# Kernel tuning notes

Hardware: AMD Instinct MI355X
Metric: run time of the kernel (lower is better)

The kernel has to match this reference:

```python
import jax, jax.numpy as jnp
import numpy as np

M, B, D, Z, CH, K = 3, 8192, 2000, 256, 2, 40
F = Z // CH  # 128


def setup_inputs() -> dict:
    key = jax.random.key(0)
    ks = jax.random.split(key, 10)
    x = jax.random.normal(ks[0], (M, B, D), jnp.float32)
    # Stacked per-modality encoder weights (Linear+ReLU stack, dropout=0)
    enc_w0 = jax.random.normal(ks[1], (M, D, 1024), jnp.float32) * 0.02
    enc_b0 = jnp.zeros((M, 1024), jnp.float32)
    enc_w1 = jax.random.normal(ks[2], (M, 1024, 512), jnp.float32) * 0.02
    enc_b1 = jnp.zeros((M, 512), jnp.float32)
    enc_w2 = jax.random.normal(ks[3], (M, 512, Z), jnp.float32) * 0.02
    enc_b2 = jnp.zeros((M, Z), jnp.float32)
    # Attention params (torch.randn init in the original)
    aff = jax.random.normal(ks[4], (3, F, F), jnp.float32)      # C(3)=3 bilinear mats
    W = jax.random.normal(ks[5], (M, K, F), jnp.float32)
    Wh = jax.random.normal(ks[6], (M, M, K, 1), jnp.float32)
    return dict(x=x, enc_w0=enc_w0, enc_b0=enc_b0, enc_w1=enc_w1, enc_b1=enc_b1,
                enc_w2=enc_w2, enc_b2=enc_b2, aff=aff, W=W, Wh=Wh)


def reference(x, enc_w0, enc_b0, enc_w1, enc_b1, enc_w2, enc_b2, aff, W, Wh):
    # Encoders: Linear+ReLU x3, batched over modalities
    h = jax.nn.relu(jnp.einsum('mbd,mdh->mbh', x, enc_w0) + enc_b0[:, None, :])
    h = jax.nn.relu(jnp.einsum('mbd,mdh->mbh', h, enc_w1) + enc_b1[:, None, :])
    z = jax.nn.relu(jnp.einsum('mbd,mdh->mbh', h, enc_w2) + enc_b2[:, None, :])  # (M,B,Z)
    m, b = z.shape[0], z.shape[1]
    t = z.reshape(m, b, F, CH)  # (M,B,128,2), same layout as torch reshape

    # aff_weight index bookkeeping exactly as the original python loops:
    # per-row i, index starts at 0 and increments only after an i<j use.
    aff_idx = {}
    for i in range(m):
        idx = 0
        for j in range(i, m):
            aff_idx[(i, j)] = idx
            if i < j:
                idx += 1

    # affinity[i][j] = t_i^T @ aff @ t_j  -> (B,CH,CH)
    afm = {}
    for i in range(m):
        for j in range(i, m):
            afm[(i, j)] = jnp.einsum('bfc,fg,bgd->bcd', t[i], aff[aff_idx[(i, j)]], t[j])

    Wt = jnp.einsum('mkf,mbfc->mbkc', W, t)  # W[i] @ t_i, (M,B,K,CH)

    H = {}
    for i in range(m):
        for j in range(m):
            if i <= j:
                H[(i, j)] = jnp.tanh(Wt[j] + jnp.einsum('bkc,bcd->bkd', Wt[i], afm[(i, j)]))
            else:
                aff_ij = jnp.swapaxes(afm[(j, i)], 1, 2)
                H[(i, j)] = jnp.tanh(Wt[i] + jnp.einsum('bkc,bcd->bkd', Wt[j], aff_ij))

    outs = []
    for i in range(m):
        for j in range(m):
            if i != j:
                # A = softmax(W_h^T @ H) over the channel axis -> (B,CH)
                a = jax.nn.softmax(jnp.einsum('k,bkc->bc', Wh[i, j, :, 0], H[(i, j)]), axis=-1)
                outs.append((a[:, None, :] * t[i]).reshape(b, Z))
    concat_data = jnp.concatenate(outs, axis=1)  # (B, M*(M-1)*Z)
    return z, concat_data
```

## Files before the change

kernel.cpp:

```cpp
#include <hip/hip_runtime.h>

#define DEVI __device__ __forceinline__

typedef _Float16 f16;
typedef _Float16 f16x8 __attribute__((ext_vector_type(8)));
typedef float f32x4 __attribute__((ext_vector_type(4)));
typedef unsigned int u32;
typedef unsigned long long u64;

#define MM 3
#define BBATCH 8192
#define DDIM 2000
#define ZDIM 256
#define KATT 40
#define K0P 2048
#define N0 1024
#define N1 512
#define N2 256

typedef __attribute__((address_space(1))) u32 gu32;
typedef __attribute__((address_space(3))) u32 lu32;

DEVI void async16(const void* g, void* l) {
  __builtin_amdgcn_global_load_lds((const gu32*)g, (lu32*)l, 16, 0, 0);
}

__global__ void k_convx(const float* __restrict__ x, f16* __restrict__ xh) {
  const long long nch = (long long)MM * BBATCH * (K0P / 8);
  for (long long idx = (long long)blockIdx.x * blockDim.x + threadIdx.x; idx < nch;
       idx += (long long)gridDim.x * blockDim.x) {
    int c8 = (int)(idx & 255);
    long long row = idx >> 8;
    union { f16 h[8]; f16x8 v; } u;
    if (c8 < DDIM / 8) {
      const float* src = x + row * DDIM + c8 * 8;
      float4 a = *reinterpret_cast<const float4*>(src);
      float4 b = *reinterpret_cast<const float4*>(src + 4);
      u.h[0] = (f16)a.x; u.h[1] = (f16)a.y; u.h[2] = (f16)a.z; u.h[3] = (f16)a.w;
      u.h[4] = (f16)b.x; u.h[5] = (f16)b.y; u.h[6] = (f16)b.z; u.h[7] = (f16)b.w;
    } else {
      for (int j = 0; j < 8; ++j) u.h[j] = (f16)0.f;
    }
    *reinterpret_cast<f16x8*>(xh + row * K0P + c8 * 8) = u.v;
  }
}

__global__ void k_wt(const float* __restrict__ w, f16* __restrict__ wt, int K, int Kpad, int N) {
  __shared__ float tile[32][33];
  int m = blockIdx.z;
  int k0 = blockIdx.x * 32, n0 = blockIdx.y * 32;
  const float* wm = w + (long long)m * K * N;
  f16* wtm = wt + (long long)m * N * Kpad;
  for (int p = 0; p < 4; ++p) {
    int idx = threadIdx.x + p * 256;
    int kk = idx >> 5, nn = idx & 31;
    float v = 0.f;
    if (k0 + kk < K) v = wm[(long long)(k0 + kk) * N + n0 + nn];
    tile[kk][nn] = v;
  }
  __syncthreads();
  for (int p = 0; p < 4; ++p) {
    int idx = threadIdx.x + p * 256;
    int nn = idx >> 5, kk = idx & 31;
    wtm[(long long)(n0 + nn) * Kpad + k0 + kk] = (f16)tile[kk][nn];
  }
}

__global__ void k_convsmall(const float* __restrict__ aff, const float* __restrict__ W,
                            f16* __restrict__ affH, f16* __restrict__ WH) {
  int idx = blockIdx.x * 256 + threadIdx.x;
  if (idx < 2 * 128 * 128) affH[idx] = (f16)aff[idx];
  if (idx < 3 * 64 * 128) {
    int m = idx >> 13;
    int k = (idx >> 7) & 63;
    int f = idx & 127;
    WH[idx] = (k < KATT) ? (f16)W[(m * KATT + k) * 128 + f] : (f16)0.f;
  }
}

template <int OUTF16>
__global__ __launch_bounds__(256, 2) void k_gemm(const f16* __restrict__ A,
                                                 const f16* __restrict__ BT,
                                                 const float* __restrict__ bias,
                                                 f16* __restrict__ outh,
                                                 float* __restrict__ outf,
                                                 f16* __restrict__ tH, int K, int N) {
  __shared__ f16 As[128 * 64];
  __shared__ f16 Bs[128 * 64];
  const int m = blockIdx.z;
  const int gm0 = blockIdx.y * 128;
  const int gn0 = blockIdx.x * 128;
  const int tid = threadIdx.x;
  const int wave = tid >> 6, lane = tid & 63;
  const int wr = wave >> 1, wc = wave & 1;

  const f16* Am = A + (long long)m * BBATCH * K;
  const f16* Bm = BT + (long long)m * N * K;

  const int srow = wave * 32 + (lane >> 3);
  const int sslot = (lane & 7) ^ (lane >> 3);
  const f16* aSrc = Am + (long long)(gm0 + srow) * K + sslot * 8;
  const f16* bSrc = Bm + (long long)(gn0 + srow) * K + sslot * 8;
  char* AsB = (char*)As;
  char* BsB = (char*)Bs;

  f32x4 zero = {0.f, 0.f, 0.f, 0.f};
  f32x4 acc[4][4];
  for (int i = 0; i < 4; ++i)
    for (int j = 0; j < 4; ++j) acc[i][j] = zero;

  for (int kt = 0; kt < K; kt += 64) {
    if (kt) __syncthreads();
#pragma unroll
    for (int q = 0; q < 4; ++q) {
      async16(aSrc + (long long)q * 8 * K + kt, AsB + (wave * 32 + q * 8) * 128);
      async16(bSrc + (long long)q * 8 * K + kt, BsB + (wave * 32 + q * 8) * 128);
    }
    __syncthreads();
#pragma unroll
    for (int ks = 0; ks < 2; ++ks) {
      f16x8 af[4], bf[4];
#pragma unroll
      for (int i = 0; i < 4; ++i) {
        int row = wr * 64 + i * 16 + (lane & 15);
        int slot = (ks * 4 + (lane >> 4)) ^ (row & 7);
        af[i] = *reinterpret_cast<const f16x8*>(AsB + row * 128 + slot * 16);
      }
#pragma unroll
      for (int j = 0; j < 4; ++j) {
        int row = wc * 64 + j * 16 + (lane & 15);
        int slot = (ks * 4 + (lane >> 4)) ^ (row & 7);
        bf[j] = *reinterpret_cast<const f16x8*>(BsB + row * 128 + slot * 16);
      }
#pragma unroll
      for (int i = 0; i < 4; ++i)
#pragma unroll
        for (int j = 0; j < 4; ++j)
          acc[i][j] = __builtin_amdgcn_mfma_f32_16x16x32_f16(af[i], bf[j], acc[i][j], 0, 0, 0);
    }
  }

  const int rowl = (lane >> 4) * 4;
  const int coll = lane & 15;
  for (int j = 0; j < 4; ++j) {
    int col = gn0 + wc * 64 + j * 16 + coll;
    float bv = bias[m * N + col];
    for (int i = 0; i < 4; ++i) {
      int row0 = gm0 + wr * 64 + i * 16 + rowl;
      for (int r = 0; r < 4; ++r) {
        float v = acc[i][j][r] + bv;
        v = v > 0.f ? v : 0.f;
        if constexpr (OUTF16) {
          outh[((long long)m * BBATCH + row0 + r) * N + col] = (f16)v;
        } else {
          outf[((long long)m * BBATCH + row0 + r) * N + col] = v;
          tH[((long long)(m * BBATCH + row0 + r) * 2 + (col & 1)) * 128 + (col >> 1)] = (f16)v;
        }
      }
    }
  }
}

__global__ __launch_bounds__(256, 2) void k_sg(const f16* __restrict__ tH,
                                               const f16* __restrict__ affH,
                                               const f16* __restrict__ WH,
                                               f16* __restrict__ u, float* __restrict__ WtG) {
  __shared__ f16 As[128 * 128];
  __shared__ f16 Bs[128 * 128];
  const int zb = blockIdx.z;
  const int gm0 = blockIdx.y * 128;
  const bool isU = (zb < 3);
  const int p = isU ? zb : zb - 3;
  const int src = isU ? ((p == 0) ? 1 : 2) : p;
  const f16* Am = tH + (long long)src * 16384 * 128;
  const f16* Bm;
  int brows;
  if (isU) {
    int km = (p == 1) ? 1 : 0;
    Bm = affH + km * 128 * 128;
    brows = 128;
  } else {
    Bm = WH + p * 64 * 128;
    brows = 64;
  }

  const int tid = threadIdx.x;
  const int wave = tid >> 6, lane = tid & 63;
  const int wr = wave >> 1, wc = wave & 1;
  char* AsB = (char*)As;
  char* BsB = (char*)Bs;

#pragma unroll
  for (int q = 0; q < 8; ++q) {
    int sb = q * 4 + wave;
    int row = sb * 4 + (lane >> 4);
    int lsl = (lane & 15) ^ (row & 7);
    async16(Am + (long long)(gm0 + row) * 128 + lsl * 8, AsB + sb * 1024);
    if (sb * 4 < brows)
      async16(Bm + (long long)row * 128 + lsl * 8, BsB + sb * 1024);
  }
  if (brows == 64) {
    f16x8 z8 = {};
    for (int idx = tid; idx < 1024; idx += 256) {
      int row = 64 + (idx >> 4), sl = idx & 15;
      *reinterpret_cast<f16x8*>(BsB + row * 256 + sl * 16) = z8;
    }
  }
  __syncthreads();

  f32x4 zero = {0.f, 0.f, 0.f, 0.f};
  f32x4 acc[4][4];
  for (int i = 0; i < 4; ++i)
    for (int j = 0; j < 4; ++j) acc[i][j] = zero;

#pragma unroll
  for (int ks = 0; ks < 4; ++ks) {
    f16x8 af[4], bf[4];
#pragma unroll
    for (int i = 0; i < 4; ++i) {
      int row = wr * 64 + i * 16 + (lane & 15);
      int slot = (ks * 4 + (lane >> 4)) ^ (row & 7);
      af[i] = *reinterpret_cast<const f16x8*>(AsB + row * 256 + slot * 16);
    }
#pragma unroll
    for (int j = 0; j < 4; ++j) {
      int row = wc * 64 + j * 16 + (lane & 15);
      int slot = (ks * 4 + (lane >> 4)) ^ (row & 7);
      bf[j] = *reinterpret_cast<const f16x8*>(BsB + row * 256 + slot * 16);
    }
#pragma unroll
    for (int i = 0; i < 4; ++i)
#pragma unroll
      for (int j = 0; j < 4; ++j)
        acc[i][j] = __builtin_amdgcn_mfma_f32_16x16x32_f16(af[i], bf[j], acc[i][j], 0, 0, 0);
  }

  const int rowl = (lane >> 4) * 4;
  const int coll = lane & 15;
  if (isU) {
    for (int j = 0; j < 4; ++j) {
      int col = wc * 64 + j * 16 + coll;
      for (int i = 0; i < 4; ++i) {
        int row0 = gm0 + wr * 64 + i * 16 + rowl;
        for (int r = 0; r < 4; ++r)
          u[((long long)p * 16384 + row0 + r) * 128 + col] = (f16)acc[i][j][r];
      }
    }
  } else if (wc == 0) {
    for (int j = 0; j < 4; ++j) {
      int col = j * 16 + coll;
      for (int i = 0; i < 4; ++i) {
        int row0 = gm0 + wr * 64 + i * 16 + rowl;
        for (int r = 0; r < 4; ++r)
          WtG[((long long)p * 16384 + row0 + r) * 64 + col] = acc[i][j][r];
      }
    }
  }
}

DEVI float dot128(const f16* __restrict__ a, const f16* __restrict__ b) {
  float s = 0.f;
#pragma unroll
  for (int ch = 0; ch < 16; ++ch) {
    f16x8 av = *reinterpret_cast<const f16x8*>(a + ch * 8);
    f16x8 bv = *reinterpret_cast<const f16x8*>(b + ch * 8);
#pragma unroll
    for (int q = 0; q < 8; ++q) s += (float)av[q] * (float)bv[q];
  }
  return s;
}

DEVI float ftanh(float x) {
  x = fminf(fmaxf(x, -15.f), 15.f);
  float t = __expf(-2.f * x);
  return (1.f - t) / (1.f + t);
}

#define BB 32
__global__ void k_tail(const float* __restrict__ z, const f16* __restrict__ tH,
                       const f16* __restrict__ u, const float* __restrict__ WtG,
                       const float* __restrict__ Wh, float* __restrict__ out) {
  __shared__ float aa[BB][6][2];
  const int tid = threadIdx.x;
  const int bbase = blockIdx.x * BB;

  if (tid < BB * 6) {
    int bb = tid / 6, q = tid % 6;
    int b = bbase + bb;
    int i = q >> 1;
    int j = (q & 1) ? ((i == 2) ? 1 : 2) : ((i == 0) ? 1 : 0);
    int a = i < j ? i : j;
    int b2 = i < j ? j : i;
    int pidx = a + b2 - 1;
    bool trans = (i > j);

    float afm[2][2];
#pragma unroll
    for (int c = 0; c < 2; ++c)
#pragma unroll
      for (int d = 0; d < 2; ++d)
        afm[c][d] = dot128(tH + ((long long)(a * BBATCH + b) * 2 + c) * 128,
                           u + ((long long)pidx * 16384 + b * 2 + d) * 128);

    float m00, m01, m10, m11;
    if (!trans) { m00 = afm[0][0]; m01 = afm[0][1]; m10 = afm[1][0]; m11 = afm[1][1]; }
    else        { m00 = afm[0][0]; m01 = afm[1][0]; m10 = afm[0][1]; m11 = afm[1][1]; }

    const float* wb0 = WtG + ((long long)b2 * 16384 + b * 2 + 0) * 64;
    const float* wb1 = WtG + ((long long)b2 * 16384 + b * 2 + 1) * 64;
    const float* wa0 = WtG + ((long long)a * 16384 + b * 2 + 0) * 64;
    const float* wa1 = WtG + ((long long)a * 16384 + b * 2 + 1) * 64;
    const float* wh = Wh + (i * 3 + j) * KATT;
    float s0 = 0.f, s1 = 0.f;
    for (int k = 0; k < KATT; ++k) {
      float a0v = wa0[k], a1v = wa1[k];
      float h0 = ftanh(wb0[k] + a0v * m00 + a1v * m10);
      float h1 = ftanh(wb1[k] + a0v * m01 + a1v * m11);
      float w = wh[k];
      s0 += w * h0;
      s1 += w * h1;
    }
    float mx = fmaxf(s0, s1);
    float e0 = __expf(s0 - mx), e1 = __expf(s1 - mx);
    float inv = 1.f / (e0 + e1);
    aa[bb][q][0] = e0 * inv;
    aa[bb][q][1] = e1 * inv;
  }
  __syncthreads();

  for (int idx = tid; idx < BB * 6 * 256; idx += 256) {
    int zz = idx & 255;
    int r = idx >> 8;
    int q = r % 6;
    int bb = r / 6;
    int iM = q >> 1;
    float av = aa[bb][q][zz & 1];
    float tv = z[((long long)iM * BBATCH + bbase + bb) * ZDIM + zz];
    out[(long long)(bbase + bb) * 1536 + q * 256 + zz] = av * tv;
  }
}

extern "C" void kernel_launch(void* const* d_in, const int* in_sizes, int n_in, void* d_out,
                              int out_size, void* d_ws, size_t ws_size, hipStream_t stream) {
  const float* x = (const float*)d_in[0];
  const float* w0 = (const float*)d_in[1];
  const float* b0 = (const float*)d_in[2];
  const float* w1 = (const float*)d_in[3];
  const float* b1 = (const float*)d_in[4];
  const float* w2 = (const float*)d_in[5];
  const float* b2 = (const float*)d_in[6];
  const float* aff = (const float*)d_in[7];
  const float* W = (const float*)d_in[8];
  const float* Wh = (const float*)d_in[9];
  float* zout = (float*)d_out;
  float* cout = zout + (long long)MM * BBATCH * ZDIM;

  char* ws = (char*)d_ws;
  size_t off = 0;
  auto alloc = [&](size_t bytes) {
    char* p = ws + off;
    off += (bytes + 255) & ~(size_t)255;
    return p;
  };
  f16* xh = (f16*)alloc((size_t)MM * BBATCH * K0P * 2);
  f16* wT0 = (f16*)alloc((size_t)MM * N0 * K0P * 2);
  f16* wT1 = (f16*)alloc((size_t)MM * N1 * N0 * 2);
  f16* wT2 = (f16*)alloc((size_t)MM * N2 * N1 * 2);
  f16* h0 = (f16*)alloc((size_t)MM * BBATCH * N0 * 2);
  f16* h1 = (f16*)alloc((size_t)MM * BBATCH * N1 * 2);
  f16* affH = (f16*)alloc((size_t)2 * 128 * 128 * 2);
  f16* WH = (f16*)alloc((size_t)3 * 64 * 128 * 2);
  if (ws_size < off) return;

  f16* tH = (f16*)xh;
  f16* u = (f16*)((char*)xh + (size_t)3 * 16384 * 128 * 2);
  float* WtG = (float*)((char*)xh + (size_t)2 * 3 * 16384 * 128 * 2);

  k_convx<<<4096, 256, 0, stream>>>(x, xh);
  k_convsmall<<<128, 256, 0, stream>>>(aff, W, affH, WH);
  k_wt<<<dim3(K0P / 32, N0 / 32, 3), 256, 0, stream>>>(w0, wT0, DDIM, K0P, N0);
  k_wt<<<dim3(N0 / 32, N1 / 32, 3), 256, 0, stream>>>(w1, wT1, N0, N0, N1);
  k_wt<<<dim3(N1 / 32, N2 / 32, 3), 256, 0, stream>>>(w2, wT2, N1, N1, N2);
  k_gemm<1><<<dim3(N0 / 128, BBATCH / 128, 3), 256, 0, stream>>>(xh, wT0, b0, h0, nullptr, nullptr, K0P, N0);
  k_gemm<1><<<dim3(N1 / 128, BBATCH / 128, 3), 256, 0, stream>>>(h0, wT1, b1, h1, nullptr, nullptr, N0, N1);
  k_gemm<0><<<dim3(N2 / 128, BBATCH / 128, 3), 256, 0, stream>>>(h1, wT2, b2, nullptr, zout, tH, N1, N2);
  k_sg<<<dim3(1, 128, 6), 256, 0, stream>>>(tH, affH, WH, u, WtG);
  k_tail<<<256, 256, 0, stream>>>(zout, tH, u, WtG, Wh, cout);
}
```

Baseline: 314.3 us.

## Add 256x128-tile triple-buffered GEMM with 8 waves and XCD-aware block swizzle

Adds a new encoder GEMM kernel that uses 512 threads and a 256x128 output tile. Global-to-LDS loads are triple-buffered and split into two phases that interleave with MFMA compute under barriers and priority hints. Block indices are remapped so that adjacent tiles land on the same XCD, which should improve L2 reuse. The aim is to hide memory latency and raise MFMA utilisation in the three dense layers. In exchange it needs 144KB of dynamic LDS, which limits occupancy, and it keeps the old kernel as a fallback in case the attribute set fails.

```diff
diff --git a/kernel.cpp b/kernel.cpp
--- a/kernel.cpp
+++ b/kernel.cpp
@@ -147,6 +147,145 @@
     float bv = bias[m * N + col];
     for (int i = 0; i < 4; ++i) {
       int row0 = gm0 + wr * 64 + i * 16 + rowl;
+      for (int r = 0; r < 4; ++r) {
+        float v = acc[i][j][r] + bv;
+        v = v > 0.f ? v : 0.f;
+        if constexpr (OUTF16) {
+          outh[((long long)m * BBATCH + row0 + r) * N + col] = (f16)v;
+        } else {
+          outf[((long long)m * BBATCH + row0 + r) * N + col] = v;
+          tH[((long long)(m * BBATCH + row0 + r) * 2 + (col & 1)) * 128 + (col >> 1)] = (f16)v;
+        }
+      }
+    }
+  }
+}
+
+template <int OUTF16>
+__global__ __launch_bounds__(512, 2) void k_gemm3(const f16* __restrict__ A,
+                                                  const f16* __restrict__ BT,
+                                                  const float* __restrict__ bias,
+                                                  f16* __restrict__ outh,
+                                                  float* __restrict__ outf,
+                                                  f16* __restrict__ tH, int K, int N) {
+  extern __shared__ char lds[];
+  const int lin = blockIdx.x + gridDim.x * (blockIdx.y + gridDim.y * blockIdx.z);
+  const int cpx = (gridDim.x * gridDim.y * gridDim.z) >> 3;
+  const int swz = (lin & 7) * cpx + (lin >> 3);
+  const int bx = swz % gridDim.x;
+  const int rest = swz / gridDim.x;
+  const int by = rest % gridDim.y;
+  const int m = rest / gridDim.y;
+
+  const int gm0 = by * 256;
+  const int gn0 = bx * 128;
+  const int tid = threadIdx.x;
+  const int wave = tid >> 6, lane = tid & 63;
+  const int wr = wave >> 2, wcq = wave & 3;
+  (void)wr; (void)wcq;
+  const int wR = wave >> 1;
+  const int wC = wave & 1;
+
+  const f16* Am = A + (long long)m * BBATCH * K;
+  const f16* Bm = BT + (long long)m * N * K;
+
+  const int srow = tid >> 3;
+  const int slog = (tid & 7) ^ (srow & 7);
+  const f16* aSrc = Am + (long long)(gm0 + srow) * K + slog * 8;
+  const f16* bSrc = Bm + (long long)(gn0 + srow) * K + slog * 8;
+
+  auto stageA = [&](int bq, int kt) {
+    char* rg = lds + bq * 49152;
+#pragma unroll
+    for (int p = 0; p < 3; ++p)
+      async16(aSrc + (long long)p * 64 * K + kt, rg + p * 8192 + wave * 1024);
+  };
+  auto stageB = [&](int bq, int kt) {
+    char* rg = lds + bq * 49152;
+    async16(aSrc + (long long)3 * 64 * K + kt, rg + 3 * 8192 + wave * 1024);
+#pragma unroll
+    for (int p = 0; p < 2; ++p)
+      async16(bSrc + (long long)p * 64 * K + kt, rg + 32768 + p * 8192 + wave * 1024);
+  };
+  auto ldA = [&](const char* buf, int i, int ks) -> f16x8 {
+    int row = wR * 64 + i * 16 + (lane & 15);
+    int slot = (ks * 4 + (lane >> 4)) ^ (row & 7);
+    return *reinterpret_cast<const f16x8*>(buf + row * 128 + slot * 16);
+  };
+  auto ldB = [&](const char* buf, int j, int ks) -> f16x8 {
+    int row = wC * 64 + j * 16 + (lane & 15);
+    int slot = (ks * 4 + (lane >> 4)) ^ (row & 7);
+    return *reinterpret_cast<const f16x8*>(buf + 32768 + row * 128 + slot * 16);
+  };
+
+  f32x4 zero = {0.f, 0.f, 0.f, 0.f};
+  f32x4 acc[4][4];
+#pragma unroll
+  for (int i = 0; i < 4; ++i)
+#pragma unroll
+    for (int j = 0; j < 4; ++j) acc[i][j] = zero;
+
+  const int NT = K >> 6;
+  stageA(0, 0); stageB(0, 0);
+  stageA(1, 64); stageB(1, 64);
+  asm volatile("s_waitcnt vmcnt(6)" ::: "memory");
+  __builtin_amdgcn_s_barrier();
+
+  for (int t = 0; t < NT; ++t) {
+    const char* buf = lds + (t % 3) * 49152;
+    const int bq2 = (t + 2) % 3;
+    const int kt2 = (t + 2) << 6;
+    const bool st = (t + 2 < NT);
+    f16x8 bf[2][4], af[2][2];
+#pragma unroll
+    for (int ks = 0; ks < 2; ++ks) {
+#pragma unroll
+      for (int j = 0; j < 4; ++j) bf[ks][j] = ldB(buf, j, ks);
+#pragma unroll
+      for (int i = 0; i < 2; ++i) af[ks][i] = ldA(buf, i, ks);
+    }
+    if (st) stageA(bq2, kt2);
+    __builtin_amdgcn_s_barrier();
+    __builtin_amdgcn_s_setprio(1);
+#pragma unroll
+    for (int ks = 0; ks < 2; ++ks)
+#pragma unroll
+      for (int i = 0; i < 2; ++i)
+#pragma unroll
+        for (int j = 0; j < 4; ++j)
+          acc[i][j] = __builtin_amdgcn_mfma_f32_16x16x32_f16(af[ks][i], bf[ks][j], acc[i][j], 0, 0, 0);
+    __builtin_amdgcn_s_setprio(0);
+    __builtin_amdgcn_s_barrier();
+#pragma unroll
+    for (int ks = 0; ks < 2; ++ks)
+#pragma unroll
+      for (int i = 0; i < 2; ++i) af[ks][i] = ldA(buf, 2 + i, ks);
+    if (st) stageB(bq2, kt2);
+    __builtin_amdgcn_s_barrier();
+    __builtin_amdgcn_s_setprio(1);
+#pragma unroll
+    for (int ks = 0; ks < 2; ++ks)
+#pragma unroll
+      for (int i = 0; i < 2; ++i)
+#pragma unroll
+        for (int j = 0; j < 4; ++j)
+          acc[2 + i][j] = __builtin_amdgcn_mfma_f32_16x16x32_f16(af[ks][i], bf[ks][j], acc[2 + i][j], 0, 0, 0);
+    __builtin_amdgcn_s_setprio(0);
+    if (t < NT - 2) {
+      asm volatile("s_waitcnt vmcnt(6)" ::: "memory");
+    } else if (t == NT - 2) {
+      asm volatile("s_waitcnt vmcnt(0)" ::: "memory");
+    }
+    __builtin_amdgcn_s_barrier();
+  }
+
+  const int rowl = (lane >> 4) * 4;
+  const int coll = lane & 15;
+  for (int j = 0; j < 4; ++j) {
+    int col = gn0 + wC * 64 + j * 16 + coll;
+    float bv = bias[m * N + col];
+    for (int i = 0; i < 4; ++i) {
+      int row0 = gm0 + wR * 64 + i * 16 + rowl;
       for (int r = 0; r < 4; ++r) {
         float v = acc[i][j][r] + bv;
         v = v > 0.f ? v : 0.f;
@@ -381,9 +520,22 @@
   k_wt<<<dim3(K0P / 32, N0 / 32, 3), 256, 0, stream>>>(w0, wT0, DDIM, K0P, N0);
   k_wt<<<dim3(N0 / 32, N1 / 32, 3), 256, 0, stream>>>(w1, wT1, N0, N0, N1);
   k_wt<<<dim3(N1 / 32, N2 / 32, 3), 256, 0, stream>>>(w2, wT2, N1, N1, N2);
-  k_gemm<1><<<dim3(N0 / 128, BBATCH / 128, 3), 256, 0, stream>>>(xh, wT0, b0, h0, nullptr, nullptr, K0P, N0);
-  k_gemm<1><<<dim3(N1 / 128, BBATCH / 128, 3), 256, 0, stream>>>(h0, wT1, b1, h1, nullptr, nullptr, N0, N1);
-  k_gemm<0><<<dim3(N2 / 128, BBATCH / 128, 3), 256, 0, stream>>>(h1, wT2, b2, nullptr, zout, tH, N1, N2);
+
+  const int LDS3 = 3 * 49152;
+  static_assert(3 * 49152 <= 160 * 1024, "LDS budget");
+  hipError_t e1 = hipFuncSetAttribute(reinterpret_cast<const void*>(&k_gemm3<1>),
+                                      hipFuncAttributeMaxDynamicSharedMemorySize, LDS3);
+  hipError_t e2 = hipFuncSetAttribute(reinterpret_cast<const void*>(&k_gemm3<0>),
+                                      hipFuncAttributeMaxDynamicSharedMemorySize, LDS3);
+  if (e1 == hipSuccess && e2 == hipSuccess) {
+    k_gemm3<1><<<dim3(N0 / 128, BBATCH / 256, 3), 512, LDS3, stream>>>(xh, wT0, b0, h0, nullptr, nullptr, K0P, N0);
+    k_gemm3<1><<<dim3(N1 / 128, BBATCH / 256, 3), 512, LDS3, stream>>>(h0, wT1, b1, h1, nullptr, nullptr, N0, N1);
+    k_gemm3<0><<<dim3(N2 / 128, BBATCH / 256, 3), 512, LDS3, stream>>>(h1, wT2, b2, nullptr, zout, tH, N1, N2);
+  } else {
+    k_gemm<1><<<dim3(N0 / 128, BBATCH / 128, 3), 256, 0, stream>>>(xh, wT0, b0, h0, nullptr, nullptr, K0P, N0);
+    k_gemm<1><<<dim3(N1 / 128, BBATCH / 128, 3), 256, 0, stream>>>(h0, wT1, b1, h1, nullptr, nullptr, N0, N1);
+    k_gemm<0><<<dim3(N2 / 128, BBATCH / 128, 3), 256, 0, stream>>>(h1, wT2, b2, nullptr, zout, tH, N1, N2);
+  }
   k_sg<<<dim3(1, 128, 6), 256, 0, stream>>>(tH, affH, WH, u, WtG);
   k_tail<<<256, 256, 0, stream>>>(zout, tH, u, WtG, Wh, cout);
 }
```

Result: faster. 305.6 us (-2.8%).

## Add 256x256-tile eight-wave pipelined GEMM for encoder layers

Applied to the files above, without the earlier changes.

Adds a new encoder GEMM kernel with 256x256 output tiles and 512 threads. It uses 128KB of double-buffered dynamic LDS filled by async global-to-LDS loads, split into four staged quarter-phases with MFMA priority boosts. Block indices are swizzled across XCDs, and the three modalities are folded into the grid's y dimension. The goal is more data reuse per tile and better overlap of loads with matrix math. The cost is fewer blocks per layer, notably only 96 blocks for the last layer, and heavy LDS and register use that limits occupancy. The old kernel stays as a fallback if setting the LDS attribute fails.

```diff
diff --git a/kernel.cpp b/kernel.cpp
--- a/kernel.cpp
+++ b/kernel.cpp
@@ -155,6 +155,156 @@
         } else {
           outf[((long long)m * BBATCH + row0 + r) * N + col] = v;
           tH[((long long)(m * BBATCH + row0 + r) * 2 + (col & 1)) * 128 + (col >> 1)] = (f16)v;
+        }
+      }
+    }
+  }
+}
+
+
+#define LDA_FRAGS(QM)                                                            \
+  _Pragma("unroll") for (int ks = 0; ks < 2; ++ks)                               \
+  _Pragma("unroll") for (int mf = 0; mf < 4; ++mf) {                             \
+    const int row_ = (QM)*128 + wrB + mf * 16 + lrow;                            \
+    af[ks][mf] = *reinterpret_cast<const f16x8*>(bufA + row_ * 128 + sl16[ks]);  \
+  }
+
+#define LDB_FRAGS(QN)                                                            \
+  _Pragma("unroll") for (int ks = 0; ks < 2; ++ks)                               \
+  _Pragma("unroll") for (int nf = 0; nf < 2; ++nf) {                             \
+    const int row_ = (QN)*128 + wcB + nf * 16 + lrow;                            \
+    bf[ks][QN][nf] = *reinterpret_cast<const f16x8*>(bufB + row_ * 128 + sl16[ks]); \
+  }
+
+#define DO_MFMA(QI, QN)                                                          \
+  __builtin_amdgcn_s_setprio(1);                                                 \
+  _Pragma("unroll") for (int ks = 0; ks < 2; ++ks)                               \
+  _Pragma("unroll") for (int mf = 0; mf < 4; ++mf)                               \
+  _Pragma("unroll") for (int nf = 0; nf < 2; ++nf)                               \
+    acc[QI][mf * 2 + nf] = __builtin_amdgcn_mfma_f32_16x16x32_f16(                \
+        af[ks][mf], bf[ks][QN][nf], acc[QI][mf * 2 + nf], 0, 0, 0);              \
+  __builtin_amdgcn_s_setprio(0);
+
+#define SYNCV(VMN)                                         \
+  asm volatile("s_waitcnt vmcnt(" #VMN ")" ::: "memory");  \
+  __builtin_amdgcn_s_barrier();
+
+#define LGKM0                                              \
+  asm volatile("s_waitcnt lgkmcnt(0)" ::: "memory");       \
+  __builtin_amdgcn_sched_barrier(0);
+
+#define ENDBAR __builtin_amdgcn_s_barrier();
+
+template <int OUTF16>
+__global__ __launch_bounds__(512, 2) void k_gemm8(const f16* __restrict__ A,
+                                                  const f16* __restrict__ BT,
+                                                  const float* __restrict__ bias,
+                                                  f16* __restrict__ outh,
+                                                  float* __restrict__ outf,
+                                                  f16* __restrict__ tH, int K, int N) {
+  extern __shared__ char lds[];
+  const int lin = blockIdx.y * gridDim.x + blockIdx.x;
+  const int cpx = (gridDim.x * gridDim.y) >> 3;
+  const int swz = (lin & 7) * cpx + (lin >> 3);
+  const int bx = swz % gridDim.x;
+  const int byy = swz / gridDim.x;
+  const int m = byy >> 5;
+  const int gm0 = (byy & 31) * 256;
+  const int gn0 = bx * 256;
+
+  const int tid = threadIdx.x;
+  const int wave = tid >> 6, lane = tid & 63;
+  const int wrB = (wave >> 2) * 64;
+  const int wcB = (wave & 3) * 32;
+  const int lrow = lane & 15;
+  int sl16[2];
+#pragma unroll
+  for (int ks = 0; ks < 2; ++ks) sl16[ks] = (((ks * 4) + (lane >> 4)) ^ (lane & 7)) * 16;
+
+  const f16* Am = A + (long long)m * BBATCH * K;
+  const f16* Bm = BT + (long long)m * N * K;
+  const int srow = tid >> 3;
+  const int slog = (tid & 7) ^ (srow & 7);
+
+  auto stage = [&](int t, int hsel) {
+    const int isB = (hsel == 1 || hsel == 2) ? 1 : 0;
+    const int h = (hsel == 2 || hsel == 3) ? 1 : 0;
+    const long long grow = (long long)(isB ? gn0 : gm0) + h * 128 + srow;
+    const f16* src = (isB ? Bm : Am) + grow * K + ((long long)t << 6) + slog * 8;
+    char* dst = lds + ((t & 1) << 16) + isB * 32768 + h * 16384 + srow * 128 + (tid & 7) * 16;
+    async16(src, dst);
+    async16(src + (long long)64 * K, dst + 8192);
+  };
+
+  f16x8 af[2][4];
+  f16x8 bf[2][2][2];
+  f32x4 acc[4][8];
+  f32x4 zero = {0.f, 0.f, 0.f, 0.f};
+#pragma unroll
+  for (int qi = 0; qi < 4; ++qi)
+#pragma unroll
+    for (int f = 0; f < 8; ++f) acc[qi][f] = zero;
+
+  const int NT = K >> 6;
+  stage(0, 0); stage(0, 1); stage(0, 2); stage(0, 3);
+
+  for (int t = 0; t < NT - 1; ++t) {
+    const char* bufA = lds + ((t & 1) << 16);
+    const char* bufB = bufA + 32768;
+    stage(t + 1, 0);
+    SYNCV(6)
+    LDA_FRAGS(0) LDB_FRAGS(0) LGKM0
+    DO_MFMA(0, 0) ENDBAR
+    stage(t + 1, 1);
+    SYNCV(6)
+    LDB_FRAGS(1) LGKM0
+    DO_MFMA(1, 1) ENDBAR
+    stage(t + 1, 2);
+    SYNCV(6)
+    LDA_FRAGS(1) LGKM0
+    DO_MFMA(2, 1) ENDBAR
+    stage(t + 1, 3);
+    DO_MFMA(3, 0)
+  }
+  {
+    const int t = NT - 1;
+    const char* bufA = lds + ((t & 1) << 16);
+    const char* bufB = bufA + 32768;
+    SYNCV(4)
+    LDA_FRAGS(0) LDB_FRAGS(0) LGKM0
+    DO_MFMA(0, 0) ENDBAR
+    SYNCV(2)
+    LDB_FRAGS(1) LGKM0
+    DO_MFMA(1, 1) ENDBAR
+    SYNCV(0)
+    LDA_FRAGS(1) LGKM0
+    DO_MFMA(2, 1) ENDBAR
+    DO_MFMA(3, 0)
+  }
+
+  const int rowl = (lane >> 4) * 4;
+  const int coll = lane & 15;
+#pragma unroll
+  for (int qi = 0; qi < 4; ++qi) {
+    const int qm = (qi >= 2) ? 1 : 0;
+    const int qn = (qi == 1 || qi == 2) ? 1 : 0;
+#pragma unroll
+    for (int nf = 0; nf < 2; ++nf) {
+      int col = gn0 + qn * 128 + wcB + nf * 16 + coll;
+      float bv = bias[m * N + col];
+#pragma unroll
+      for (int mf = 0; mf < 4; ++mf) {
+        int row0 = gm0 + qm * 128 + wrB + mf * 16 + rowl;
+#pragma unroll
+        for (int r = 0; r < 4; ++r) {
+          float v = acc[qi][mf * 2 + nf][r] + bv;
+          v = v > 0.f ? v : 0.f;
+          if constexpr (OUTF16) {
+            outh[((long long)m * BBATCH + row0 + r) * N + col] = (f16)v;
+          } else {
+            outf[((long long)m * BBATCH + row0 + r) * N + col] = v;
+            tH[((long long)(m * BBATCH + row0 + r) * 2 + (col & 1)) * 128 + (col >> 1)] = (f16)v;
+          }
         }
       }
     }
@@ -381,9 +531,21 @@
   k_wt<<<dim3(K0P / 32, N0 / 32, 3), 256, 0, stream>>>(w0, wT0, DDIM, K0P, N0);
   k_wt<<<dim3(N0 / 32, N1 / 32, 3), 256, 0, stream>>>(w1, wT1, N0, N0, N1);
   k_wt<<<dim3(N1 / 32, N2 / 32, 3), 256, 0, stream>>>(w2, wT2, N1, N1, N2);
-  k_gemm<1><<<dim3(N0 / 128, BBATCH / 128, 3), 256, 0, stream>>>(xh, wT0, b0, h0, nullptr, nullptr, K0P, N0);
-  k_gemm<1><<<dim3(N1 / 128, BBATCH / 128, 3), 256, 0, stream>>>(h0, wT1, b1, h1, nullptr, nullptr, N0, N1);
-  k_gemm<0><<<dim3(N2 / 128, BBATCH / 128, 3), 256, 0, stream>>>(h1, wT2, b2, nullptr, zout, tH, N1, N2);
+
+  const int LDS8 = 2 * 65536;
+  hipError_t e1 = hipFuncSetAttribute(reinterpret_cast<const void*>(&k_gemm8<1>),
+                                      hipFuncAttributeMaxDynamicSharedMemorySize, LDS8);
+  hipError_t e2 = hipFuncSetAttribute(reinterpret_cast<const void*>(&k_gemm8<0>),
+                                      hipFuncAttributeMaxDynamicSharedMemorySize, LDS8);
+  if (e1 == hipSuccess && e2 == hipSuccess) {
+    k_gemm8<1><<<dim3(N0 / 256, 96), 512, LDS8, stream>>>(xh, wT0, b0, h0, nullptr, nullptr, K0P, N0);
+    k_gemm8<1><<<dim3(N1 / 256, 96), 512, LDS8, stream>>>(h0, wT1, b1, h1, nullptr, nullptr, N0, N1);
+    k_gemm8<0><<<dim3(N2 / 256, 96), 512, LDS8, stream>>>(h1, wT2, b2, nullptr, zout, tH, N1, N2);
+  } else {
+    k_gemm<1><<<dim3(N0 / 128, BBATCH / 128, 3), 256, 0, stream>>>(xh, wT0, b0, h0, nullptr, nullptr, K0P, N0);
+    k_gemm<1><<<dim3(N1 / 128, BBATCH / 128, 3), 256, 0, stream>>>(h0, wT1, b1, h1, nullptr, nullptr, N0, N1);
+    k_gemm<0><<<dim3(N2 / 128, BBATCH / 128, 3), 256, 0, stream>>>(h1, wT2, b2, nullptr, zout, tH, N1, N2);
+  }
   k_sg<<<dim3(1, 128, 6), 256, 0, stream>>>(tH, affH, WH, u, WtG);
   k_tail<<<256, 256, 0, stream>>>(zout, tH, u, WtG, Wh, cout);
 }
```

Result: faster. 304.6 us (-3.1%).

## Add triple-buffered 256x128 MFMA GEMM with ping-pong fragment pipeline for encoders

Applied to the files above, without the earlier changes.

Adds a new encoder GEMM kernel with 512 threads and 256x128 output tiles. It stages three K-tiles in dynamic LDS (about 147KB) using async global-to-LDS loads with an XOR swizzle. LDS fragment reads are double-buffered in registers, interleaved with MFMA bursts under raised wave priority, and a block-index swizzle improves cache locality. The aim is to hide global and LDS latency behind matrix math and raise MFMA use in the three encoder GEMMs. The cost is a large LDS footprint that limits occupancy to one block per CU, and the old kernel is kept as a fallback if the LDS attribute cannot be set.

```diff
diff --git a/kernel.cpp b/kernel.cpp
--- a/kernel.cpp
+++ b/kernel.cpp
@@ -149,6 +149,165 @@
       int row0 = gm0 + wr * 64 + i * 16 + rowl;
       for (int r = 0; r < 4; ++r) {
         float v = acc[i][j][r] + bv;
+        v = v > 0.f ? v : 0.f;
+        if constexpr (OUTF16) {
+          outh[((long long)m * BBATCH + row0 + r) * N + col] = (f16)v;
+        } else {
+          outf[((long long)m * BBATCH + row0 + r) * N + col] = v;
+          tH[((long long)(m * BBATCH + row0 + r) * 2 + (col & 1)) * 128 + (col >> 1)] = (f16)v;
+        }
+      }
+    }
+  }
+}
+
+
+#define SYNCV(VMN)                                         \
+  asm volatile("s_waitcnt vmcnt(" #VMN ")" ::: "memory");  \
+  __builtin_amdgcn_s_barrier();
+
+#define LGKM8                                              \
+  asm volatile("s_waitcnt lgkmcnt(8)" ::: "memory");       \
+  __builtin_amdgcn_sched_barrier(0);
+
+#define LGKM0F                                             \
+  asm volatile("s_waitcnt lgkmcnt(0)" ::: "memory");       \
+  __builtin_amdgcn_sched_barrier(0);
+
+#define ENDBAR __builtin_amdgcn_s_barrier();
+
+#define RD1(D, BUFP, OFF)                                                     \
+  {                                                                           \
+    u32 a_ = (u32)(unsigned long)(lu32*)((BUFP) + (OFF));                     \
+    asm volatile("ds_read_b128 %0, %1" : "=v"(D) : "v"(a_));                  \
+  }
+
+#define READ8(FR, BUFP, KS)                                                   \
+  RD1(FR[0], BUFP, offA##KS[0]) RD1(FR[1], BUFP, offA##KS[1])                 \
+  RD1(FR[2], BUFP, offA##KS[2]) RD1(FR[3], BUFP, offA##KS[3])                 \
+  RD1(FR[4], BUFP, offB##KS[0]) RD1(FR[5], BUFP, offB##KS[1])                 \
+  RD1(FR[6], BUFP, offB##KS[2]) RD1(FR[7], BUFP, offB##KS[3])
+
+#define MFMA16(FR)                                                            \
+  __builtin_amdgcn_s_setprio(1);                                              \
+  _Pragma("unroll") for (int mf = 0; mf < 4; ++mf)                            \
+  _Pragma("unroll") for (int nf = 0; nf < 4; ++nf)                            \
+    acc[mf][nf] = __builtin_amdgcn_mfma_f32_16x16x32_f16(                     \
+        FR[mf], FR[4 + nf], acc[mf][nf], 0, 0, 0);                            \
+  __builtin_amdgcn_s_setprio(0);
+
+template <int OUTF16>
+__global__ __launch_bounds__(512, 2) void k_gemmp(const f16* __restrict__ A,
+                                                  const f16* __restrict__ BT,
+                                                  const float* __restrict__ bias,
+                                                  f16* __restrict__ outh,
+                                                  float* __restrict__ outf,
+                                                  f16* __restrict__ tH, int K, int N) {
+  extern __shared__ char lds[];
+  const int lin = blockIdx.y * gridDim.x + blockIdx.x;
+  const int cpx = (gridDim.x * gridDim.y) >> 3;
+  const int swz = (lin & 7) * cpx + (lin >> 3);
+  const int bx = swz % gridDim.x;
+  const int byy = swz / gridDim.x;
+  const int m = byy >> 5;
+  const int gm0 = (byy & 31) * 256;
+  const int gn0 = bx * 128;
+
+  const int tid = threadIdx.x;
+  const int wave = tid >> 6, lane = tid & 63;
+  const int wR = wave >> 1;
+  const int wC = wave & 1;
+  const int lrow = lane & 15;
+  const int l4 = lane >> 4;
+
+  const f16* Am = A + (long long)m * BBATCH * K;
+  const f16* Bm = BT + (long long)m * N * K;
+  const int srow = tid >> 3;
+  const int slog = (tid & 7) ^ (srow & 7);
+
+  auto stage3 = [&](int t, int h) {
+    char* buf = lds + (t % 3) * 49152;
+    const long long kt = (long long)t << 6;
+    const f16* sa = Am + (long long)(gm0 + h * 128 + srow) * K + kt + slog * 8;
+    char* da = buf + (h * 128 + srow) * 128 + (tid & 7) * 16;
+    async16(sa, da);
+    async16(sa + (long long)64 * K, da + 64 * 128);
+    const f16* sb = Bm + (long long)(gn0 + h * 64 + srow) * K + kt + slog * 8;
+    async16(sb, buf + 32768 + (h * 64 + srow) * 128 + (tid & 7) * 16);
+  };
+
+  u32 offA0[4], offA1[4], offB0[4], offB1[4];
+#pragma unroll
+  for (int mf = 0; mf < 4; ++mf) {
+    int ra = wR * 64 + mf * 16 + lrow;
+    offA0[mf] = ra * 128 + (((0 + l4) ^ (ra & 7)) << 4);
+    offA1[mf] = ra * 128 + (((4 + l4) ^ (ra & 7)) << 4);
+    int rb = wC * 64 + mf * 16 + lrow;
+    offB0[mf] = 32768 + rb * 128 + (((0 + l4) ^ (rb & 7)) << 4);
+    offB1[mf] = 32768 + rb * 128 + (((4 + l4) ^ (rb & 7)) << 4);
+  }
+
+  f16x8 frA[8], frB[8];
+  f32x4 acc[4][4];
+  f32x4 zero = {0.f, 0.f, 0.f, 0.f};
+#pragma unroll
+  for (int i = 0; i < 4; ++i)
+#pragma unroll
+    for (int j = 0; j < 4; ++j) acc[i][j] = zero;
+
+  const int NT = K >> 6;
+  stage3(0, 0); stage3(0, 1); stage3(1, 0); stage3(1, 1);
+  SYNCV(6)
+  { char* b0 = lds; READ8(frA, b0, 0) }
+
+  for (int t = 0; t <= NT - 3; ++t) {
+    char* bufC = lds + (t % 3) * 49152;
+    char* bufN = lds + ((t + 1) % 3) * 49152;
+    stage3(t + 2, 0);
+    SYNCV(6)
+    READ8(frB, bufC, 1)
+    LGKM8
+    MFMA16(frA)
+    ENDBAR
+    stage3(t + 2, 1);
+    SYNCV(6)
+    READ8(frA, bufN, 0)
+    LGKM8
+    MFMA16(frB)
+    ENDBAR
+  }
+  {
+    char* bufC = lds + ((NT - 2) % 3) * 49152;
+    char* bufN = lds + ((NT - 1) % 3) * 49152;
+    SYNCV(3)
+    READ8(frB, bufC, 1)
+    LGKM8
+    MFMA16(frA)
+    ENDBAR
+    SYNCV(0)
+    READ8(frA, bufN, 0)
+    LGKM8
+    MFMA16(frB)
+    ENDBAR
+    READ8(frB, bufN, 1)
+    LGKM8
+    MFMA16(frA)
+    LGKM0F
+    MFMA16(frB)
+  }
+
+  const int rowl = (lane >> 4) * 4;
+  const int coll = lane & 15;
+#pragma unroll
+  for (int nf = 0; nf < 4; ++nf) {
+    int col = gn0 + wC * 64 + nf * 16 + coll;
+    float bv = bias[m * N + col];
+#pragma unroll
+    for (int mf = 0; mf < 4; ++mf) {
+      int row0 = gm0 + wR * 64 + mf * 16 + rowl;
+#pragma unroll
+      for (int r = 0; r < 4; ++r) {
+        float v = acc[mf][nf][r] + bv;
         v = v > 0.f ? v : 0.f;
         if constexpr (OUTF16) {
           outh[((long long)m * BBATCH + row0 + r) * N + col] = (f16)v;
@@ -381,9 +540,21 @@
   k_wt<<<dim3(K0P / 32, N0 / 32, 3), 256, 0, stream>>>(w0, wT0, DDIM, K0P, N0);
   k_wt<<<dim3(N0 / 32, N1 / 32, 3), 256, 0, stream>>>(w1, wT1, N0, N0, N1);
   k_wt<<<dim3(N1 / 32, N2 / 32, 3), 256, 0, stream>>>(w2, wT2, N1, N1, N2);
-  k_gemm<1><<<dim3(N0 / 128, BBATCH / 128, 3), 256, 0, stream>>>(xh, wT0, b0, h0, nullptr, nullptr, K0P, N0);
-  k_gemm<1><<<dim3(N1 / 128, BBATCH / 128, 3), 256, 0, stream>>>(h0, wT1, b1, h1, nullptr, nullptr, N0, N1);
-  k_gemm<0><<<dim3(N2 / 128, BBATCH / 128, 3), 256, 0, stream>>>(h1, wT2, b2, nullptr, zout, tH, N1, N2);
+
+  const int LDSP = 3 * 49152;
+  hipError_t e1 = hipFuncSetAttribute(reinterpret_cast<const void*>(&k_gemmp<1>),
+                                      hipFuncAttributeMaxDynamicSharedMemorySize, LDSP);
+  hipError_t e2 = hipFuncSetAttribute(reinterpret_cast<const void*>(&k_gemmp<0>),
+                                      hipFuncAttributeMaxDynamicSharedMemorySize, LDSP);
+  if (e1 == hipSuccess && e2 == hipSuccess) {
+    k_gemmp<1><<<dim3(N0 / 128, 96), 512, LDSP, stream>>>(xh, wT0, b0, h0, nullptr, nullptr, K0P, N0);
+    k_gemmp<1><<<dim3(N1 / 128, 96), 512, LDSP, stream>>>(h0, wT1, b1, h1, nullptr, nullptr, N0, N1);
+    k_gemmp<0><<<dim3(N2 / 128, 96), 512, LDSP, stream>>>(h1, wT2, b2, nullptr, zout, tH, N1, N2);
+  } else {
+    k_gemm<1><<<dim3(N0 / 128, BBATCH / 128, 3), 256, 0, stream>>>(xh, wT0, b0, h0, nullptr, nullptr, K0P, N0);
+    k_gemm<1><<<dim3(N1 / 128, BBATCH / 128, 3), 256, 0, stream>>>(h0, wT1, b1, h1, nullptr, nullptr, N0, N1);
+    k_gemm<0><<<dim3(N2 / 128, BBATCH / 128, 3), 256, 0, stream>>>(h1, wT2, b2, nullptr, zout, tH, N1, N2);
+  }
   k_sg<<<dim3(1, 128, 6), 256, 0, stream>>>(tH, affH, WH, u, WtG);
   k_tail<<<256, 256, 0, stream>>>(zout, tH, u, WtG, Wh, cout);
 }
```

Result: faster. 307.4 us (-2.2%).
